# Kernel tuning notes

Measured on AMD Instinct MI355X. Metric: run time of the kernel, lower is better.

The kernel has to match this reference:

```python
import jax, jax.numpy as jnp
import numpy as np

NUM_HEADS = 16
HEAD_DIM = 128
WINDOW = 512
ROPE_BASE = 10000.0


def _rope_tables(seq_len, head_dim, dtype=jnp.float32):
    # rotate_dim == head_dim (rope_proportion=1.0)
    inv_freq = 1.0 / (ROPE_BASE ** (jnp.arange(0, head_dim, 2, dtype=jnp.float32) / head_dim))
    freqs = jnp.arange(seq_len, dtype=jnp.float32)[:, None] * inv_freq[None, :]  # (S, D/2)
    return jnp.cos(freqs).astype(dtype), jnp.sin(freqs).astype(dtype)


def _apply_rope(x, cos, sin):
    # x: (B, H, S, D); interleaved-pair RoPE matching torch reference
    x1 = x[..., 0::2]
    x2 = x[..., 1::2]
    cos = cos[None, None]  # (1,1,S,D/2)
    sin = sin[None, None]
    re = x1 * cos - x2 * sin
    ro = x1 * sin + x2 * cos
    out = jnp.stack([re, ro], axis=-1)  # (B,H,S,D/2,2)
    return out.reshape(x.shape)


def setup_inputs() -> dict:
    key = jax.random.key(0)
    ks = jax.random.split(key, 5)
    B, S, D = 2, 2048, 2048
    std = 0.02
    x = jax.random.normal(ks[0], (B, S, D), dtype=jnp.float32)
    Wq = std * jax.random.normal(ks[1], (D, D), dtype=jnp.float32)
    Wk = std * jax.random.normal(ks[2], (D, D), dtype=jnp.float32)
    Wv = std * jax.random.normal(ks[3], (D, D), dtype=jnp.float32)
    Wo = std * jax.random.normal(ks[4], (D, D), dtype=jnp.float32)
    return {"x": x, "Wq": Wq, "Wk": Wk, "Wv": Wv, "Wo": Wo}


def reference(x, Wq, Wk, Wv, Wo):
    B, S, D = x.shape
    H, Dh = NUM_HEADS, HEAD_DIM
    scale = Dh ** -0.5

    def to_heads(t):
        return t.reshape(B, S, H, Dh).transpose(0, 2, 1, 3)  # (B,H,S,Dh)

    q = to_heads(x @ Wq.T)
    k = to_heads(x @ Wk.T)
    v = to_heads(x @ Wv.T)

    cos, sin = _rope_tables(S, Dh)
    q = _apply_rope(q, cos, sin)
    k = _apply_rope(k, cos, sin)

    # sliding-window causal mask: keep if 0 <= row-col < WINDOW
    pos = jnp.arange(S)
    diff = pos[:, None] - pos[None, :]
    keep = (diff >= 0) & (diff < WINDOW)  # (S,S) bool

    scores = jnp.einsum('bhsd,bhtd->bhst', q, k) * scale
    scores = jnp.where(keep[None, None], scores, jnp.finfo(scores.dtype).min)
    attn = jax.nn.softmax(scores, axis=-1)
    out = jnp.einsum('bhst,bhtd->bhsd', attn, v)  # (B,H,S,Dh)
    out = out.transpose(0, 2, 1, 3).reshape(B, S, D)
    return out @ Wo.T
```

## Files before the change

kernel.cpp:

```cpp
#include <hip/hip_runtime.h>
#include <cstdint>
#include <cstddef>

typedef __bf16 bf16x8 __attribute__((ext_vector_type(8)));
typedef float f32x4 __attribute__((ext_vector_type(4)));
typedef float f32x16 __attribute__((ext_vector_type(16)));
typedef unsigned int u32x2v __attribute__((ext_vector_type(2)));
typedef unsigned short u16;

constexpr int S_LEN  = 2048;
constexpr int DMODEL = 2048;
constexpr int NHEAD  = 16;
constexpr int HDIM   = 128;
constexpr int WIN    = 512;

#define AS1 __attribute__((address_space(1)))
#define AS3 __attribute__((address_space(3)))
#define BAR() do { asm volatile("" ::: "memory"); __builtin_amdgcn_s_barrier(); asm volatile("" ::: "memory"); } while (0)
#define WAITVM(n) asm volatile("s_waitcnt vmcnt(" #n ")" ::: "memory")

__device__ __forceinline__ u16 f2bf(float f) {
  union { float ff; uint32_t u; } a; a.ff = f;
  return (u16)((a.u + 0x7fffu + ((a.u >> 16) & 1u)) >> 16);
}

__device__ __forceinline__ uint32_t cvtpk(float lo, float hi) {
  uint32_t r;
  asm("v_cvt_pk_bf16_f32 %0, %1, %2" : "=v"(r) : "v"(lo), "v"(hi));
  return r;
}

__global__ void cvt_all(const float* __restrict__ x,  const float* __restrict__ wq,
                        const float* __restrict__ wk, const float* __restrict__ wv,
                        const float* __restrict__ wo,
                        u16* __restrict__ xb,  u16* __restrict__ wqb,
                        u16* __restrict__ wkb, u16* __restrict__ wvb,
                        u16* __restrict__ wob) {
  const int total = 6291456;
  int i = blockIdx.x * blockDim.x + threadIdx.x;
  const int stride = gridDim.x * blockDim.x;
  for (; i < total; i += stride) {
    const int r = i >> 20;
    const float* src; u16* dst; int off;
    if (r < 2)       { src = x;  dst = xb;  off = i; }
    else if (r == 2) { src = wq; dst = wqb; off = i - (2 << 20); }
    else if (r == 3) { src = wk; dst = wkb; off = i - (3 << 20); }
    else if (r == 4) { src = wv; dst = wvb; off = i - (4 << 20); }
    else             { src = wo; dst = wob; off = i - (5 << 20); }
    float4 v = reinterpret_cast<const float4*>(src)[off];
    uint2 pk;
    pk.x = (uint32_t)f2bf(v.x) | ((uint32_t)f2bf(v.y) << 16);
    pk.y = (uint32_t)f2bf(v.z) | ((uint32_t)f2bf(v.w) << 16);
    reinterpret_cast<uint2*>(dst)[off] = pk;
  }
}

__global__ void rope_kernel(float* __restrict__ rc, float* __restrict__ rs) {
  const int i = blockIdx.x * blockDim.x + threadIdx.x;
  const int s = i >> 6, f = i & 63;
  const double inv = exp(-(double)f * (log(10000.0) / 64.0));
  const double a = (double)s * inv;
  rc[i] = (float)cos(a);
  rs[i] = (float)sin(a);
}

__global__ __launch_bounds__(256, 2)
void gemm_qkv192(const u16* __restrict__ A, const u16* __restrict__ Bcat,
                 u16* __restrict__ qout, u16* __restrict__ kout, u16* __restrict__ vtout,
                 const float* __restrict__ rc, const float* __restrict__ rs) {
  constexpr int K = DMODEL;
  constexpr int NH = K / 32;
  __shared__ __align__(16) u16 sm[4 * 10240];

  const int ct = blockIdx.x, mt = blockIdx.y;
  const int brow = mt * 128;
  const int bcol = ct * 192;

  const int tid = threadIdx.x;
  const int w = tid >> 6, lane = tid & 63;
  const int lr = lane & 15, lk = lane >> 4;
  const int wm = w >> 1, wn = w & 1;

  const u16* Ag = A    + (size_t)brow * K;
  const u16* Bg = Bcat + (size_t)bcol * K;

  f32x4 acc[4][6] = {};

  auto stage = [&](int h) {
    const int sb = (h & 3) * 10240;
#pragma unroll
    for (int i = 0; i < 2; ++i) {
      const int u = i * 256 + tid;
      const int rf = u >> 6, lkk = (u >> 4) & 3, lrr = u & 15;
      const u16* src = Ag + (size_t)(rf * 16 + lrr) * K + h * 32 + lkk * 8;
      __builtin_amdgcn_global_load_lds((const AS1 void*)src,
          (AS3 void*)(&sm[sb + (i * 256 + w * 64) * 8]), 16, 0, 0);
    }
#pragma unroll
    for (int i = 0; i < 3; ++i) {
      const int u = i * 256 + tid;
      const int cf = u >> 6, lkk = (u >> 4) & 3, lrr = u & 15;
      const u16* src = Bg + (size_t)(cf * 16 + lrr) * K + h * 32 + lkk * 8;
      __builtin_amdgcn_global_load_lds((const AS1 void*)src,
          (AS3 void*)(&sm[sb + (512 + i * 256 + w * 64) * 8]), 16, 0, 0);
    }
  };

  stage(0); stage(1); stage(2);
  WAITVM(10);
  BAR();

  for (int h = 0; h < NH; ++h) {
    const int sb = (h & 3) * 10240;
    bf16x8 a[4], b[6];
#pragma unroll
    for (int mf = 0; mf < 4; ++mf)
      a[mf] = *reinterpret_cast<const bf16x8*>(&sm[sb + (((wm * 4 + mf) * 4 + lk) * 16 + lr) * 8]);
#pragma unroll
    for (int nf = 0; nf < 6; ++nf)
      b[nf] = *reinterpret_cast<const bf16x8*>(&sm[sb + (512 + ((wn * 6 + nf) * 4 + lk) * 16 + lr) * 8]);
    if (h + 3 < NH) stage(h + 3);
    BAR();
    __builtin_amdgcn_s_setprio(1);
#pragma unroll
    for (int mf = 0; mf < 4; ++mf)
#pragma unroll
      for (int nf = 0; nf < 6; ++nf)
        acc[mf][nf] = __builtin_amdgcn_mfma_f32_16x16x32_bf16(a[mf], b[nf], acc[mf][nf], 0, 0, 0);
    __builtin_amdgcn_s_setprio(0);
    if (h < NH - 3)       { WAITVM(10); }
    else if (h == NH - 3) { WAITVM(5); }
    else if (h == NH - 2) { WAITVM(0); }
    BAR();
  }

#pragma unroll
  for (int mf = 0; mf < 4; ++mf) {
    const int gm0 = brow + wm * 64 + mf * 16 + lk * 4;
    const int b_ = gm0 >> 11, s0 = gm0 & 2047;
#pragma unroll
    for (int nf = 0; nf < 6; ++nf) {
      const int gn = bcol + wn * 96 + nf * 16 + lr;
      const int reg = gn >> 11;
      const int h = (gn >> 7) & 15, dh = gn & 127;
      if (reg == 2) {
        uint2 pk;
        pk.x = (uint32_t)f2bf(acc[mf][nf][0]) | ((uint32_t)f2bf(acc[mf][nf][1]) << 16);
        pk.y = (uint32_t)f2bf(acc[mf][nf][2]) | ((uint32_t)f2bf(acc[mf][nf][3]) << 16);
        *reinterpret_cast<uint2*>(&vtout[((size_t)((b_ * NHEAD + h) * HDIM + dh)) * S_LEN + s0]) = pk;
      } else {
        u16* QK = reg == 0 ? qout : kout;
        const int fi = dh >> 1;
        const bool ev = (dh & 1) == 0;
#pragma unroll
        for (int j = 0; j < 4; ++j) {
          float v = acc[mf][nf][j];
          float pp = __shfl_xor(v, 1, 64);
          const float c  = rc[(s0 + j) * 64 + fi];
          const float sn = rs[(s0 + j) * 64 + fi];
          float oo = ev ? (v * c - pp * sn) : (pp * sn + v * c);
          if (reg == 0) oo *= 0.08838834764831845f;
          QK[((size_t)(b_ * NHEAD + h) * S_LEN + (s0 + j)) * HDIM + dh] = f2bf(oo);
        }
      }
    }
  }
}

__global__ __launch_bounds__(256, 2)
void gemm_o(const u16* __restrict__ A, const u16* __restrict__ Bw,
            float* __restrict__ O) {
  constexpr int K = DMODEL;
  constexpr int BK = 64;
  __shared__ __align__(16) u16 As[128 * BK];
  __shared__ __align__(16) u16 Bs[128 * BK];
  const int tid = threadIdx.x;
  const int w = tid >> 6, lane = tid & 63;
  const int lr = lane & 15, lk = lane >> 4;
  const int wm = w >> 1, wn = w & 1;
  const int brow = blockIdx.y * 128;
  const int bcol = blockIdx.x * 128;

  f32x4 acc[4][4] = {};

  const int st_row = w * 32 + (lane >> 3);
  const int st_col = (lane & 7) * 8;
  const u16* Ag = A  + (size_t)(brow + st_row) * K + st_col;
  const u16* Bg = Bw + (size_t)(bcol + st_row) * K + st_col;
  u16* AsW = As + w * 32 * BK;
  u16* BsW = Bs + w * 32 * BK;

  for (int k0 = 0; k0 < K; k0 += BK) {
#pragma unroll
    for (int i = 0; i < 4; ++i)
      __builtin_amdgcn_global_load_lds(
          (const AS1 void*)(Ag + (size_t)i * 8 * K + k0),
          (AS3 void*)(AsW + i * 8 * BK), 16, 0, 0);
#pragma unroll
    for (int i = 0; i < 4; ++i)
      __builtin_amdgcn_global_load_lds(
          (const AS1 void*)(Bg + (size_t)i * 8 * K + k0),
          (AS3 void*)(BsW + i * 8 * BK), 16, 0, 0);
    __syncthreads();
#pragma unroll
    for (int kc = 0; kc < 2; ++kc) {
      bf16x8 a[4], b[4];
#pragma unroll
      for (int m = 0; m < 4; ++m)
        a[m] = *reinterpret_cast<const bf16x8*>(&As[(wm * 64 + m * 16 + lr) * BK + kc * 32 + lk * 8]);
#pragma unroll
      for (int n = 0; n < 4; ++n)
        b[n] = *reinterpret_cast<const bf16x8*>(&Bs[(wn * 64 + n * 16 + lr) * BK + kc * 32 + lk * 8]);
#pragma unroll
      for (int m = 0; m < 4; ++m)
#pragma unroll
        for (int n = 0; n < 4; ++n)
          acc[m][n] = __builtin_amdgcn_mfma_f32_16x16x32_bf16(a[m], b[n], acc[m][n], 0, 0, 0);
    }
    __syncthreads();
  }

#pragma unroll
  for (int m = 0; m < 4; ++m) {
    const int gm0 = brow + wm * 64 + m * 16 + lk * 4;
#pragma unroll
    for (int n = 0; n < 4; ++n) {
      const int gn = bcol + wn * 64 + n * 16 + lr;
#pragma unroll
      for (int j = 0; j < 4; ++j)
        O[(size_t)(gm0 + j) * DMODEL + gn] = acc[m][n][j];
    }
  }
}

__global__ __launch_bounds__(256, 2)
void swa3_kernel(const u16* __restrict__ Qp, const u16* __restrict__ Kp,
                 const u16* __restrict__ Vt, u16* __restrict__ AO) {
  __shared__ __align__(16) u16 Ksh[2][64 * 128];
  __shared__ __align__(16) u16 Vsh[2][128 * 64];

  const int lin = blockIdx.x + gridDim.x * blockIdx.y;
  const int slot = lin >> 3;
  const int bh = (lin & 7) * 4 + (slot >> 4);
  const int qt = slot & 15;

  const int w = threadIdx.x >> 6;
  const int lane = threadIdx.x & 63;
  const int lq = lane & 31, hi = lane >> 5;
  const int qb_blk = qt * 128;
  const int qw = qb_blk + w * 32;
  const int qq = qw + lq;

  const u16* Qb = Qp + (size_t)bh * S_LEN * HDIM;
  const u16* Kb = Kp + (size_t)bh * S_LEN * HDIM;
  const u16* Vb = Vt + (size_t)bh * HDIM * S_LEN;

  bf16x8 qf[8];
#pragma unroll
  for (int s = 0; s < 8; ++s)
    qf[s] = *reinterpret_cast<const bf16x8*>(&Qb[(size_t)qq * HDIM + s * 16 + hi * 8]);

  f32x16 ot[4] = {};
  float m = 0.f, lsum = 0.f;

  const int c_lo = (qb_blk >= WIN) ? qb_blk - WIN : 0;
  const int c_hi = qb_blk + 128;

  auto stage = [&](int buf, int kc) {
#pragma unroll
    for (int i = 0; i < 4; ++i) {
      const int u = i * 256 + w * 64 + lane;
      const int row = u >> 4, sl = (u & 15) ^ (row & 7);
      __builtin_amdgcn_global_load_lds(
          (const AS1 void*)(Kb + (size_t)(kc + row) * HDIM + sl * 8),
          (AS3 void*)(&Ksh[buf][(size_t)(i * 256 + w * 64) * 8]), 16, 0, 0);
    }
#pragma unroll
    for (int i = 0; i < 4; ++i) {
      const int u = i * 256 + w * 64 + lane;
      const int row = u >> 3, sl = (u & 7) ^ (row & 7);
      __builtin_amdgcn_global_load_lds(
          (const AS1 void*)(Vb + (size_t)row * S_LEN + kc + sl * 8),
          (AS3 void*)(&Vsh[buf][(size_t)(i * 256 + w * 64) * 8]), 16, 0, 0);
    }
  };

  int buf = 0;
  stage(0, c_lo);
  __syncthreads();

  for (int kc = c_lo; kc < c_hi; kc += 64, buf ^= 1) {
    if (kc + 64 < c_hi) stage(buf ^ 1, kc + 64);

#pragma unroll
    for (int half = 0; half < 2; ++half) {
      const int kch = kc + half * 32;
      if (kch > qw + 31 || kch < qw - 542) continue;

      f32x16 P = {};
#pragma unroll
      for (int s = 0; s < 8; ++s) {
        const int row = half * 32 + lq;
        const int byte = row * 256 + ((s * 32 + hi * 16) ^ ((row & 7) << 4));
        bf16x8 kf = *reinterpret_cast<const bf16x8*>(&Ksh[buf][byte >> 1]);
        P = __builtin_amdgcn_mfma_f32_32x32x16_bf16(kf, qf[s], P, 0, 0, 0);
      }

      const bool needmask = (kch + 32 > qw) || (qw + 31 - kch >= WIN);
      float p[16];
      float pmax = -1e30f;
#pragma unroll
      for (int r = 0; r < 16; ++r) {
        float v = P[r];
        if (needmask) {
          const int kk = kch + (r & 3) + ((r >> 2) << 3) + hi * 4;
          const bool keep = (qq >= kk) && (qq - kk < WIN);
          v = keep ? v : -1e30f;
        }
        p[r] = v;
        pmax = fmaxf(pmax, v);
      }

      if (__any(pmax - m > 8.f)) {
        const float rm = fmaxf(pmax, __shfl_xor(pmax, 32, 64));
        const float mnew = fmaxf(m, rm);
        const float alpha = __expf(m - mnew);
        lsum *= alpha;
#pragma unroll
        for (int dt = 0; dt < 4; ++dt)
#pragma unroll
          for (int r = 0; r < 16; ++r) ot[dt][r] *= alpha;
        m = mnew;
      }

      float ls = 0.f;
#pragma unroll
      for (int r = 0; r < 16; ++r) {
        p[r] = __expf(p[r] - m);
        ls += p[r];
      }
      lsum += ls;

      uint32_t W[8];
#pragma unroll
      for (int i = 0; i < 8; ++i) W[i] = cvtpk(p[2 * i], p[2 * i + 1]);
      u32x2v r02 = __builtin_amdgcn_permlane32_swap(W[0], W[2], false, false);
      u32x2v r13 = __builtin_amdgcn_permlane32_swap(W[1], W[3], false, false);
      u32x2v r46 = __builtin_amdgcn_permlane32_swap(W[4], W[6], false, false);
      u32x2v r57 = __builtin_amdgcn_permlane32_swap(W[5], W[7], false, false);

#pragma unroll
      for (int ks = 0; ks < 2; ++ks) {
        union { uint32_t u[4]; bf16x8 v; } pb;
        if (ks == 0) { pb.u[0] = r02[0]; pb.u[1] = r13[0]; pb.u[2] = r02[1]; pb.u[3] = r13[1]; }
        else         { pb.u[0] = r46[0]; pb.u[1] = r57[0]; pb.u[2] = r46[1]; pb.u[3] = r57[1]; }
#pragma unroll
        for (int dt = 0; dt < 4; ++dt) {
          const int d = dt * 32 + lq;
          const int byte = d * 128 + ((half * 64 + ks * 32 + hi * 16) ^ ((d & 7) << 4));
          bf16x8 vf = *reinterpret_cast<const bf16x8*>(&Vsh[buf][byte >> 1]);
          ot[dt] = __builtin_amdgcn_mfma_f32_32x32x16_bf16(vf, pb.v, ot[dt], 0, 0, 0);
        }
      }
    }
    __syncthreads();
  }

  const float lf = lsum + __shfl_xor(lsum, 32, 64);
  const float inv = 1.f / lf;
  const int b = bh >> 4, h = bh & 15;
  u16* Ob = AO + (size_t)(b * S_LEN + qq) * DMODEL + h * HDIM;
#pragma unroll
  for (int dt = 0; dt < 4; ++dt)
#pragma unroll
    for (int rq = 0; rq < 4; ++rq) {
      uint2 pk;
      pk.x = cvtpk(ot[dt][rq * 4 + 0] * inv, ot[dt][rq * 4 + 1] * inv);
      pk.y = cvtpk(ot[dt][rq * 4 + 2] * inv, ot[dt][rq * 4 + 3] * inv);
      *reinterpret_cast<uint2*>(&Ob[dt * 32 + rq * 8 + hi * 4]) = pk;
    }
}

extern "C" void kernel_launch(void* const* d_in, const int* in_sizes, int n_in,
                              void* d_out, int out_size, void* d_ws, size_t ws_size,
                              hipStream_t stream) {
  const float* x  = (const float*)d_in[0];
  const float* Wq = (const float*)d_in[1];
  const float* Wk = (const float*)d_in[2];
  const float* Wv = (const float*)d_in[3];
  const float* Wo = (const float*)d_in[4];
  float* out = (float*)d_out;

  u16* p = (u16*)d_ws;
  u16* xb  = p; p += (size_t)4096 * 2048;
  u16* wqb = p; p += (size_t)2048 * 2048;
  u16* wkb = p; p += (size_t)2048 * 2048;
  u16* wvb = p; p += (size_t)2048 * 2048;
  u16* wob = p; p += (size_t)2048 * 2048;
  u16* qb  = p; p += (size_t)32 * 2048 * 128;
  u16* kb  = p; p += (size_t)32 * 2048 * 128;
  u16* vtb = p; p += (size_t)32 * 128 * 2048;
  u16* aob = p; p += (size_t)4096 * 2048;
  float* rc = (float*)p;
  float* rs = rc + (size_t)2048 * 64;

  cvt_all<<<3072, 256, 0, stream>>>(x, Wq, Wk, Wv, Wo, xb, wqb, wkb, wvb, wob);
  rope_kernel<<<512, 256, 0, stream>>>(rc, rs);
  gemm_qkv192<<<dim3(32, 32), 256, 0, stream>>>(xb, wqb, qb, kb, vtb, rc, rs);
  swa3_kernel<<<dim3(16, 32), 256, 0, stream>>>(qb, kb, vtb, aob);
  gemm_o<<<dim3(16, 32), 256, 0, stream>>>(aob, wob, out);
}
```

Measured before the change: 269.2 us.

## Replace multi-stage QKV pipeline with single-buffer BK=128 loop, retile gemm_o LDS

The QKV GEMM drops its 4-deep software pipeline (explicit vmcnt waits, raw barriers, setprio) for a simple loop that loads one 128-wide K slab per iteration, guarded by two __syncthreads. The output projection GEMM moves to the same fragment-major LDS layout with a 128-wide K step. The RoPE epilogue now packs even/odd pairs into 32-bit stores. Together these halve the number of loop iterations and barriers and make LDS reads conflict-free. The cost is that load/compute overlap within a block is lost and LDS use per block grows.

```diff
diff --git a/kernel.cpp b/kernel.cpp
--- a/kernel.cpp
+++ b/kernel.cpp
@@ -16,8 +16,6 @@
 
 #define AS1 __attribute__((address_space(1)))
 #define AS3 __attribute__((address_space(3)))
-#define BAR() do { asm volatile("" ::: "memory"); __builtin_amdgcn_s_barrier(); asm volatile("" ::: "memory"); } while (0)
-#define WAITVM(n) asm volatile("s_waitcnt vmcnt(" #n ")" ::: "memory")
 
 __device__ __forceinline__ u16 f2bf(float f) {
   union { float ff; uint32_t u; } a; a.ff = f;
@@ -65,12 +63,11 @@
 }
 
 __global__ __launch_bounds__(256, 2)
-void gemm_qkv192(const u16* __restrict__ A, const u16* __restrict__ Bcat,
-                 u16* __restrict__ qout, u16* __restrict__ kout, u16* __restrict__ vtout,
-                 const float* __restrict__ rc, const float* __restrict__ rs) {
+void gemm_qkv(const u16* __restrict__ A, const u16* __restrict__ Bcat,
+              u16* __restrict__ qout, u16* __restrict__ kout, u16* __restrict__ vtout,
+              const float* __restrict__ rc, const float* __restrict__ rs) {
   constexpr int K = DMODEL;
-  constexpr int NH = K / 32;
-  __shared__ __align__(16) u16 sm[4 * 10240];
+  __shared__ __align__(16) u16 sm[5120 * 8];
 
   const int ct = blockIdx.x, mt = blockIdx.y;
   const int brow = mt * 128;
@@ -86,52 +83,43 @@
 
   f32x4 acc[4][6] = {};
 
-  auto stage = [&](int h) {
-    const int sb = (h & 3) * 10240;
-#pragma unroll
-    for (int i = 0; i < 2; ++i) {
+  for (int k0 = 0; k0 < K; k0 += 128) {
+#pragma unroll
+    for (int i = 0; i < 8; ++i) {
       const int u = i * 256 + tid;
-      const int rf = u >> 6, lkk = (u >> 4) & 3, lrr = u & 15;
-      const u16* src = Ag + (size_t)(rf * 16 + lrr) * K + h * 32 + lkk * 8;
+      const int ulr = u & 15, ulk = (u >> 4) & 3, urf = (u >> 6) & 7, ukc = (u >> 9) & 3;
+      const u16* src = Ag + (size_t)(urf * 16 + ulr) * K + k0 + ukc * 32 + ulk * 8;
       __builtin_amdgcn_global_load_lds((const AS1 void*)src,
-          (AS3 void*)(&sm[sb + (i * 256 + w * 64) * 8]), 16, 0, 0);
-    }
-#pragma unroll
-    for (int i = 0; i < 3; ++i) {
+          (AS3 void*)(&sm[(i * 256 + w * 64) * 8]), 16, 0, 0);
+    }
+#pragma unroll
+    for (int i = 0; i < 12; ++i) {
       const int u = i * 256 + tid;
-      const int cf = u >> 6, lkk = (u >> 4) & 3, lrr = u & 15;
-      const u16* src = Bg + (size_t)(cf * 16 + lrr) * K + h * 32 + lkk * 8;
+      const int ulr = u & 15, ulk = (u >> 4) & 3, t = u >> 6;
+      const int ucf = t % 12, ukc = t / 12;
+      const u16* src = Bg + (size_t)(ucf * 16 + ulr) * K + k0 + ukc * 32 + ulk * 8;
       __builtin_amdgcn_global_load_lds((const AS1 void*)src,
-          (AS3 void*)(&sm[sb + (512 + i * 256 + w * 64) * 8]), 16, 0, 0);
-    }
-  };
-
-  stage(0); stage(1); stage(2);
-  WAITVM(10);
-  BAR();
-
-  for (int h = 0; h < NH; ++h) {
-    const int sb = (h & 3) * 10240;
-    bf16x8 a[4], b[6];
-#pragma unroll
-    for (int mf = 0; mf < 4; ++mf)
-      a[mf] = *reinterpret_cast<const bf16x8*>(&sm[sb + (((wm * 4 + mf) * 4 + lk) * 16 + lr) * 8]);
-#pragma unroll
-    for (int nf = 0; nf < 6; ++nf)
-      b[nf] = *reinterpret_cast<const bf16x8*>(&sm[sb + (512 + ((wn * 6 + nf) * 4 + lk) * 16 + lr) * 8]);
-    if (h + 3 < NH) stage(h + 3);
-    BAR();
-    __builtin_amdgcn_s_setprio(1);
-#pragma unroll
-    for (int mf = 0; mf < 4; ++mf)
+          (AS3 void*)(&sm[(2048 + i * 256 + w * 64) * 8]), 16, 0, 0);
+    }
+    __syncthreads();
+#pragma unroll
+    for (int kc = 0; kc < 4; ++kc) {
+      bf16x8 a[4], b[6];
+#pragma unroll
+      for (int mf = 0; mf < 4; ++mf)
+        a[mf] = *reinterpret_cast<const bf16x8*>(
+            &sm[(((kc * 8 + wm * 4 + mf) * 4 + lk) * 16 + lr) * 8]);
 #pragma unroll
       for (int nf = 0; nf < 6; ++nf)
-        acc[mf][nf] = __builtin_amdgcn_mfma_f32_16x16x32_bf16(a[mf], b[nf], acc[mf][nf], 0, 0, 0);
-    __builtin_amdgcn_s_setprio(0);
-    if (h < NH - 3)       { WAITVM(10); }
-    else if (h == NH - 3) { WAITVM(5); }
-    else if (h == NH - 2) { WAITVM(0); }
-    BAR();
+        b[nf] = *reinterpret_cast<const bf16x8*>(
+            &sm[(2048 + ((kc * 12 + wn * 6 + nf) * 4 + lk) * 16 + lr) * 8]);
+#pragma unroll
+      for (int mf = 0; mf < 4; ++mf)
+#pragma unroll
+        for (int nf = 0; nf < 6; ++nf)
+          acc[mf][nf] = __builtin_amdgcn_mfma_f32_16x16x32_bf16(a[mf], b[nf], acc[mf][nf], 0, 0, 0);
+    }
+    __syncthreads();
   }
 
 #pragma unroll
@@ -160,7 +148,12 @@
           const float sn = rs[(s0 + j) * 64 + fi];
           float oo = ev ? (v * c - pp * sn) : (pp * sn + v * c);
           if (reg == 0) oo *= 0.08838834764831845f;
-          QK[((size_t)(b_ * NHEAD + h) * S_LEN + (s0 + j)) * HDIM + dh] = f2bf(oo);
+          const float op = __shfl_xor(oo, 1, 64);
+          if (ev) {
+            const uint32_t pk = (uint32_t)f2bf(oo) | ((uint32_t)f2bf(op) << 16);
+            *reinterpret_cast<uint32_t*>(
+                &QK[((size_t)(b_ * NHEAD + h) * S_LEN + (s0 + j)) * HDIM + dh]) = pk;
+          }
         }
       }
     }
@@ -171,64 +164,68 @@
 void gemm_o(const u16* __restrict__ A, const u16* __restrict__ Bw,
             float* __restrict__ O) {
   constexpr int K = DMODEL;
-  constexpr int BK = 64;
-  __shared__ __align__(16) u16 As[128 * BK];
-  __shared__ __align__(16) u16 Bs[128 * BK];
+  __shared__ __align__(16) u16 sm[4096 * 8];
+
+  const int brow = blockIdx.y * 128;
+  const int bcol = blockIdx.x * 128;
+
   const int tid = threadIdx.x;
   const int w = tid >> 6, lane = tid & 63;
   const int lr = lane & 15, lk = lane >> 4;
   const int wm = w >> 1, wn = w & 1;
-  const int brow = blockIdx.y * 128;
-  const int bcol = blockIdx.x * 128;
+
+  const u16* Ag = A  + (size_t)brow * K;
+  const u16* Bg = Bw + (size_t)bcol * K;
 
   f32x4 acc[4][4] = {};
 
-  const int st_row = w * 32 + (lane >> 3);
-  const int st_col = (lane & 7) * 8;
-  const u16* Ag = A  + (size_t)(brow + st_row) * K + st_col;
-  const u16* Bg = Bw + (size_t)(bcol + st_row) * K + st_col;
-  u16* AsW = As + w * 32 * BK;
-  u16* BsW = Bs + w * 32 * BK;
-
-  for (int k0 = 0; k0 < K; k0 += BK) {
-#pragma unroll
-    for (int i = 0; i < 4; ++i)
-      __builtin_amdgcn_global_load_lds(
-          (const AS1 void*)(Ag + (size_t)i * 8 * K + k0),
-          (AS3 void*)(AsW + i * 8 * BK), 16, 0, 0);
-#pragma unroll
-    for (int i = 0; i < 4; ++i)
-      __builtin_amdgcn_global_load_lds(
-          (const AS1 void*)(Bg + (size_t)i * 8 * K + k0),
-          (AS3 void*)(BsW + i * 8 * BK), 16, 0, 0);
+  for (int k0 = 0; k0 < K; k0 += 128) {
+#pragma unroll
+    for (int i = 0; i < 8; ++i) {
+      const int u = i * 256 + tid;
+      const int ulr = u & 15, ulk = (u >> 4) & 3, urf = (u >> 6) & 7, ukc = (u >> 9) & 3;
+      const u16* src = Ag + (size_t)(urf * 16 + ulr) * K + k0 + ukc * 32 + ulk * 8;
+      __builtin_amdgcn_global_load_lds((const AS1 void*)src,
+          (AS3 void*)(&sm[(i * 256 + w * 64) * 8]), 16, 0, 0);
+    }
+#pragma unroll
+    for (int i = 0; i < 8; ++i) {
+      const int u = i * 256 + tid;
+      const int ulr = u & 15, ulk = (u >> 4) & 3, urf = (u >> 6) & 7, ukc = (u >> 9) & 3;
+      const u16* src = Bg + (size_t)(urf * 16 + ulr) * K + k0 + ukc * 32 + ulk * 8;
+      __builtin_amdgcn_global_load_lds((const AS1 void*)src,
+          (AS3 void*)(&sm[(2048 + i * 256 + w * 64) * 8]), 16, 0, 0);
+    }
     __syncthreads();
 #pragma unroll
-    for (int kc = 0; kc < 2; ++kc) {
+    for (int kc = 0; kc < 4; ++kc) {
       bf16x8 a[4], b[4];
 #pragma unroll
-      for (int m = 0; m < 4; ++m)
-        a[m] = *reinterpret_cast<const bf16x8*>(&As[(wm * 64 + m * 16 + lr) * BK + kc * 32 + lk * 8]);
-#pragma unroll
-      for (int n = 0; n < 4; ++n)
-        b[n] = *reinterpret_cast<const bf16x8*>(&Bs[(wn * 64 + n * 16 + lr) * BK + kc * 32 + lk * 8]);
-#pragma unroll
-      for (int m = 0; m < 4; ++m)
-#pragma unroll
-        for (int n = 0; n < 4; ++n)
-          acc[m][n] = __builtin_amdgcn_mfma_f32_16x16x32_bf16(a[m], b[n], acc[m][n], 0, 0, 0);
+      for (int mf = 0; mf < 4; ++mf)
+        a[mf] = *reinterpret_cast<const bf16x8*>(
+            &sm[(((kc * 8 + wm * 4 + mf) * 4 + lk) * 16 + lr) * 8]);
+#pragma unroll
+      for (int nf = 0; nf < 4; ++nf)
+        b[nf] = *reinterpret_cast<const bf16x8*>(
+            &sm[(2048 + ((kc * 8 + wn * 4 + nf) * 4 + lk) * 16 + lr) * 8]);
+#pragma unroll
+      for (int mf = 0; mf < 4; ++mf)
+#pragma unroll
+        for (int nf = 0; nf < 4; ++nf)
+          acc[mf][nf] = __builtin_amdgcn_mfma_f32_16x16x32_bf16(a[mf], b[nf], acc[mf][nf], 0, 0, 0);
     }
     __syncthreads();
   }
 
 #pragma unroll
-  for (int m = 0; m < 4; ++m) {
-    const int gm0 = brow + wm * 64 + m * 16 + lk * 4;
-#pragma unroll
-    for (int n = 0; n < 4; ++n) {
-      const int gn = bcol + wn * 64 + n * 16 + lr;
+  for (int mf = 0; mf < 4; ++mf) {
+    const int gm0 = brow + wm * 64 + mf * 16 + lk * 4;
+#pragma unroll
+    for (int nf = 0; nf < 4; ++nf) {
+      const int gn = bcol + wn * 64 + nf * 16 + lr;
 #pragma unroll
       for (int j = 0; j < 4; ++j)
-        O[(size_t)(gm0 + j) * DMODEL + gn] = acc[m][n][j];
+        O[(size_t)(gm0 + j) * DMODEL + gn] = acc[mf][nf][j];
     }
   }
 }
@@ -406,7 +403,7 @@
 
   cvt_all<<<3072, 256, 0, stream>>>(x, Wq, Wk, Wv, Wo, xb, wqb, wkb, wvb, wob);
   rope_kernel<<<512, 256, 0, stream>>>(rc, rs);
-  gemm_qkv192<<<dim3(32, 32), 256, 0, stream>>>(xb, wqb, qb, kb, vtb, rc, rs);
+  gemm_qkv<<<dim3(32, 32), 256, 0, stream>>>(xb, wqb, qb, kb, vtb, rc, rs);
   swa3_kernel<<<dim3(16, 32), 256, 0, stream>>>(qb, kb, vtb, aob);
   gemm_o<<<dim3(16, 32), 256, 0, stream>>>(aob, wob, out);
 }
```

Result: slower. 360.0 us (+33.7%).
